# Optimization experiments

Measured on AMD Instinct MI355X. Metric: run time of the kernel, lower is better.

The kernel has to match this reference:

```python
import jax, jax.numpy as jnp
import numpy as np

V, E, H, K, B, T = 50000, 256, 256, 9, 128, 512


def lstm_dir(x, lens, Wih, Whh, b):
    # x: [B,T,E] -> h outputs [B,T,H], packed-sequence semantics:
    # state frozen and outputs zeroed for t >= lens[b].
    Bs, Ts, _ = x.shape
    Hh = Whh.shape[1]
    xw = jnp.einsum('bte,ge->btg', x, Wih) + b  # [B,T,4H] precomputed input proj
    valid = jnp.arange(Ts)[None, :] < lens[:, None]  # [B,T]

    def step(carry, inp):
        h, c = carry
        xw_t, v = inp  # [B,4H], [B]
        gates = xw_t + h @ Whh.T
        i, f, g, o = jnp.split(gates, 4, axis=-1)  # torch gate order i,f,g,o
        i = jax.nn.sigmoid(i)
        f = jax.nn.sigmoid(f)
        g = jnp.tanh(g)
        o = jax.nn.sigmoid(o)
        c_new = f * c + i * g
        h_new = o * jnp.tanh(c_new)
        v = v[:, None]
        return (jnp.where(v, h_new, h), jnp.where(v, c_new, c)), h_new * v

    init = (jnp.zeros((Bs, Hh), x.dtype), jnp.zeros((Bs, Hh), x.dtype))
    _, ys = jax.lax.scan(step, init, (jnp.swapaxes(xw, 0, 1), valid.T))
    return jnp.swapaxes(ys, 0, 1)


def reverse_by_len(x, lens):
    # per-row reversal within valid length; padding stays zero
    Ts = x.shape[1]
    t = jnp.arange(Ts)
    idx = jnp.clip(lens[:, None] - 1 - t[None, :], 0, Ts - 1)
    m = t[None, :] < lens[:, None]
    return jnp.take_along_axis(x, idx[:, :, None], axis=1) * m[:, :, None]


def crf_llh(em, tags, lens, start, end, trans):
    # torchcrf forward with reduction='sum': sum_b (gold score - logZ)
    Bs, Ts, Kk = em.shape
    mask = jnp.arange(Ts)[None, :] < lens[:, None]
    em_t = jnp.take_along_axis(em, tags[..., None], axis=-1)[..., 0]  # [B,T]
    score = start[tags[:, 0]] + em_t[:, 0]
    tr = trans[tags[:, :-1], tags[:, 1:]]  # [B,T-1]
    score = score + jnp.sum((tr + em_t[:, 1:]) * mask[:, 1:], axis=1)
    last_tag = jnp.take_along_axis(tags, (lens - 1)[:, None], axis=1)[:, 0]
    score = score + end[last_tag]

    def step(alpha, inp):
        e_t, m_t = inp  # [B,K], [B]
        nxt = jax.nn.logsumexp(alpha[:, :, None] + trans[None, :, :], axis=1) + e_t
        return jnp.where(m_t[:, None], nxt, alpha), None

    alpha0 = start[None, :] + em[:, 0]  # [B,K]
    alpha, _ = jax.lax.scan(step, alpha0,
                            (jnp.swapaxes(em[:, 1:], 0, 1), mask[:, 1:].T))
    logZ = jax.nn.logsumexp(alpha + end[None, :], axis=1)
    return jnp.sum(score - logZ)


def setup_inputs() -> dict:
    key = jax.random.key(0)
    ks = jax.random.split(key, 16)
    sentences = jax.random.randint(ks[0], (B, T), 0, V)
    tags = jax.random.randint(ks[1], (B, T), 0, K)
    length_list = jax.random.randint(ks[2], (B,), 1, T + 1)  # >=1 so mask[:,0] all true
    s = float(1.0 / np.sqrt(H))
    u = lambda k, sh: jax.random.uniform(k, sh, jnp.float32, -s, s)
    emb = jax.random.normal(ks[3], (V, E), jnp.float32) * float(np.sqrt(2.0 / E))
    return dict(
        sentences=sentences, tags=tags, length_list=length_list,
        emb=emb,
        Wih_f=u(ks[4], (4 * H, E)), Whh_f=u(ks[5], (4 * H, H)), b_f=u(ks[6], (4 * H,)),
        Wih_b=u(ks[7], (4 * H, E)), Whh_b=u(ks[8], (4 * H, H)), b_b=u(ks[9], (4 * H,)),
        W_out=u(ks[10], (K, 2 * H)), b_out=u(ks[11], (K,)),
        start=jax.random.uniform(ks[12], (K,), jnp.float32, -0.1, 0.1),
        end=jax.random.uniform(ks[13], (K,), jnp.float32, -0.1, 0.1),
        trans=jax.random.uniform(ks[14], (K, K), jnp.float32, -0.1, 0.1),
    )


def reference(sentences, tags, length_list, emb, Wih_f, Whh_f, b_f,
              Wih_b, Whh_b, b_b, W_out, b_out, start, end, trans):
    x = emb[sentences]  # [B,T,E]
    h_f = lstm_dir(x, length_list, Wih_f, Whh_f, b_f)
    x_rev = reverse_by_len(x, length_list)
    h_b = reverse_by_len(lstm_dir(x_rev, length_list, Wih_b, Whh_b, b_b), length_list)
    hcat = jnp.concatenate([h_f, h_b], axis=-1)  # [B,T,2H]
    # Dropout is identity in eval mode
    em = jnp.einsum('bth,kh->btk', hcat, W_out) + b_out  # [B,T,K]
    return crf_llh(em, tags, length_list, start, end, trans)
```

## Files before the change

kernel.cpp:

```cpp
#include <hip/hip_runtime.h>
#include <hip/hip_bf16.h>

typedef short v8s __attribute__((ext_vector_type(8)));
typedef int   v8i __attribute__((ext_vector_type(8)));
typedef float v4f __attribute__((ext_vector_type(4)));
typedef float v2f __attribute__((ext_vector_type(2)));

#define T_ 512

template<int HI>
__device__ __forceinline__ v2f cvt2(unsigned int wsrc){
  return __builtin_amdgcn_cvt_pk_f32_fp8((int)wsrc, HI);
}
__device__ __forceinline__ v2f rcp2(v2f d){
  return (v2f){__builtin_amdgcn_rcpf(d.x), __builtin_amdgcn_rcpf(d.y)};
}
__device__ __forceinline__ v2f tanh2(v2f x){
  v2f x2 = x*x;
  v2f num = x*(x2 + 27.f);
  v2f den = x2*9.f + 27.f;
  v2f r = num * rcp2(den);
  return (v2f){__builtin_amdgcn_fmed3f(r.x,-1.f,1.f),
               __builtin_amdgcn_fmed3f(r.y,-1.f,1.f)};
}
__device__ __forceinline__ v2f sigm2(v2f x){
  v2f y = x*0.5f;
  v2f y2 = y*y;
  v2f num = y*(y2 + 27.f);
  v2f den = y2*9.f + 27.f;
  v2f r = num * rcp2(den);
  v2f rc = (v2f){__builtin_amdgcn_fmed3f(r.x,-1.f,1.f),
                 __builtin_amdgcn_fmed3f(r.y,-1.f,1.f)};
  return rc*0.5f + 0.5f;
}
__device__ __forceinline__ int pi_col(int p){
  return ((p>>5)<<5) + ((p&1)<<4) + ((p&31)>>1);
}
__device__ __forceinline__ v8i ld32(const void* p){
  uint4 lo = *(const uint4*)p;
  uint4 hi = *(const uint4*)((const char*)p + 16);
  v8i r;
  r[0]=(int)lo.x; r[1]=(int)lo.y; r[2]=(int)lo.z; r[3]=(int)lo.w;
  r[4]=(int)hi.x; r[5]=(int)hi.y; r[6]=(int)hi.z; r[7]=(int)hi.w;
  return r;
}
__device__ __forceinline__ unsigned f2fp4(float x){
  unsigned s = (x < 0.f) ? 8u : 0u;
  float a = fabsf(x);
  unsigned m;
  if      (a < 0.25f) m=0u; else if (a < 0.75f) m=1u;
  else if (a < 1.25f) m=2u; else if (a < 1.75f) m=3u;
  else if (a < 2.5f ) m=4u; else if (a < 3.5f ) m=5u;
  else if (a < 5.f  ) m=6u; else m=7u;
  return s|m;
}
__device__ __forceinline__ unsigned pk8(float a, float b, float c, float d){
  int w = __builtin_amdgcn_cvt_pk_fp8_f32(a, b, 0, 0);
  w     = __builtin_amdgcn_cvt_pk_fp8_f32(c, d, w, 1);
  return (unsigned)w;
}
__device__ __forceinline__ unsigned enc4(v2f h){
  v2f t = h*4.f;
  unsigned b = 0;
  #pragma unroll
  for (int s=0;s<2;++s){
    float v = s ? t.y : t.x;
    float ax = __builtin_amdgcn_fmed3f(fabsf(v), 0.f, 4.f);
    float gl = fmaf(ax, 2.f, 12582912.f);
    float gh = ax + 12582912.f;
    unsigned ql = __builtin_bit_cast(unsigned, gl) & 7u;
    unsigned qh = (__builtin_bit_cast(unsigned, gh) & 7u) + 2u;
    unsigned c  = (ax > 1.75f) ? qh : ql;
    unsigned sg = (__builtin_bit_cast(unsigned, v) >> 28) & 8u;
    b |= (c | sg) << (4*s);
  }
  return b;
}

__global__ __launch_bounds__(256) void prep_wih8_k(
    const float* __restrict__ Wa, const float* __restrict__ Wb,
    unsigned char* __restrict__ out)
{
  int idx = blockIdx.x*256 + threadIdx.x;
  int lane = idx & 63;
  int t2 = idx >> 6;
  int ntile = t2 & 127;
  int kt = t2 >> 7;
  int n = ntile*16 + (lane&15);
  const float* W = (n < 1024) ? (Wa + (size_t)n*256) : (Wb + (size_t)(n-1024)*256);
  int k0 = kt*128 + (lane>>4)*32;
  unsigned words[8];
  #pragma unroll
  for (int e=0;e<8;++e)
    words[e] = pk8(W[k0+e*4], W[k0+e*4+1], W[k0+e*4+2], W[k0+e*4+3]);
  unsigned char* d = out + (size_t)idx*32;
  *(uint4*)(d)      = make_uint4(words[0], words[1], words[2], words[3]);
  *(uint4*)(d + 16) = make_uint4(words[4], words[5], words[6], words[7]);
}

__global__ __launch_bounds__(256) void prep_whh4_k(
    const float* __restrict__ Wf, const float* __restrict__ Wb,
    unsigned char* __restrict__ out)
{
  int idx = blockIdx.x*256 + threadIdx.x;
  int lane = idx & 63;
  int t2 = idx >> 6;
  int ntile = t2 & 63;
  int kt = (t2>>6) & 1;
  int dir = t2 >> 7;
  const float* W = dir ? Wb : Wf;
  int n = ntile*16 + (lane&15);
  int kbase = kt*128 + (lane>>4)*32;
  const float* row = W + (size_t)n*256;
  unsigned words[4];
  #pragma unroll
  for (int d4=0;d4<4;++d4){
    unsigned acc = 0;
    #pragma unroll
    for (int j=0;j<8;++j){
      float v = row[pi_col(kbase + d4*8 + j)] * 64.f;
      acc |= f2fp4(v) << (4*j);
    }
    words[d4] = acc;
  }
  *(uint4*)(out + (size_t)idx*16) = make_uint4(words[0], words[1], words[2], words[3]);
}

__global__ __launch_bounds__(256) void xw_gemm_k(
    const int* __restrict__ sent, const float* __restrict__ emb,
    const unsigned char* __restrict__ wihg, const int* __restrict__ lens,
    const float* __restrict__ bfv, const float* __restrict__ bbv,
    unsigned char* __restrict__ xw)
{
  int mt = blockIdx.x;
  if (((mt&3)<<7) >= lens[mt>>2]) return;
  __shared__ unsigned char A[128][272];
  int tid = threadIdx.x;
  {
    int row = tid>>1, half = tid&1;
    int tok = sent[mt*128 + row];
    const float4* s = (const float4*)(emb + (size_t)tok*256 + half*128);
    unsigned char* drow = &A[row][half*128];
    #pragma unroll
    for (int c4=0; c4<8; ++c4){
      unsigned w0[4];
      #pragma unroll
      for (int u=0; u<4; ++u){
        float4 v = s[c4*4+u];
        w0[u] = pk8(v.x, v.y, v.z, v.w);
      }
      *(uint4*)(drow + c4*16) = make_uint4(w0[0], w0[1], w0[2], w0[3]);
    }
  }
  __syncthreads();
  int w = tid>>6, lane = tid&63, lr = lane&15, lq = lane>>4;
  #pragma unroll 1
  for (int i4=0; i4<4; ++i4){
    int dnv = w*4 + i4;
    int dn = dnv>>3, v = dnv&7;
    const float* bb = dn ? bbv : bfv;
    float bias[8];
    #pragma unroll
    for (int e=0;e<8;++e){
      int q = e>>1, s = e&1;
      bias[e] = bb[q*256 + v*32 + s*16 + lr];
    }
    #pragma unroll 1
    for (int mh=0; mh<2; ++mh){
      v4f acc[8][4];
      #pragma unroll
      for (int e=0;e<8;++e)
        #pragma unroll
        for (int mm=0;mm<4;++mm) acc[e][mm] = (v4f){0.f,0.f,0.f,0.f};
      #pragma unroll
      for (int kt=0;kt<2;++kt){
        v8i a0 = ld32(&A[mh*64 +  0 + lr][kt*128 + lq*32]);
        v8i a1 = ld32(&A[mh*64 + 16 + lr][kt*128 + lq*32]);
        v8i a2 = ld32(&A[mh*64 + 32 + lr][kt*128 + lq*32]);
        v8i a3 = ld32(&A[mh*64 + 48 + lr][kt*128 + lq*32]);
        #pragma unroll
        for (int e=0;e<8;++e){
          int q = e>>1, s = e&1;
          int ntile = dn*64 + q*16 + v*2 + s;
          v8i bfr = ld32(wihg + ((size_t)(kt*128 + ntile)*64 + lane)*32);
          acc[e][0] = __builtin_amdgcn_mfma_scale_f32_16x16x128_f8f6f4(
                        a0, bfr, acc[e][0], 0,0, 0,0x7f7f7f7f, 0,0x7f7f7f7f);
          acc[e][1] = __builtin_amdgcn_mfma_scale_f32_16x16x128_f8f6f4(
                        a1, bfr, acc[e][1], 0,0, 0,0x7f7f7f7f, 0,0x7f7f7f7f);
          acc[e][2] = __builtin_amdgcn_mfma_scale_f32_16x16x128_f8f6f4(
                        a2, bfr, acc[e][2], 0,0, 0,0x7f7f7f7f, 0,0x7f7f7f7f);
          acc[e][3] = __builtin_amdgcn_mfma_scale_f32_16x16x128_f8f6f4(
                        a3, bfr, acc[e][3], 0,0, 0,0x7f7f7f7f, 0,0x7f7f7f7f);
        }
      }
      #pragma unroll
      for (int mm=0;mm<4;++mm){
        #pragma unroll
        for (int j=0;j<4;++j){
          int row = mt*128 + mh*64 + mm*16 + lq*4 + j;
          unsigned lo = pk8(acc[0][mm][j]+bias[0], acc[1][mm][j]+bias[1],
                            acc[2][mm][j]+bias[2], acc[3][mm][j]+bias[3]);
          unsigned hi = pk8(acc[4][mm][j]+bias[4], acc[5][mm][j]+bias[5],
                            acc[6][mm][j]+bias[6], acc[7][mm][j]+bias[7]);
          *(uint2*)(xw + ((size_t)dn*65536 + row)*1024 + v*128 + lr*8)
              = make_uint2(lo, hi);
        }
      }
    }
  }
}

__global__ __launch_bounds__(512,1) void lstm_k(
    const unsigned char* __restrict__ xw,
    const unsigned char* __restrict__ whh4,
    const int* __restrict__ lens,
    unsigned char* __restrict__ hout)
{
  int bid = blockIdx.x, dir = bid>>5, grp = bid&31;
  int tid = threadIdx.x, w = tid>>6, lane = tid&63, lr = lane&15, lq = lane>>4;
  __shared__ unsigned char hbuf[2][16][136];
  __shared__ int tmax_s;
  for (int i=tid*4; i<2*16*136; i+=512*4) *(unsigned int*)(&((unsigned char*)hbuf)[i]) = 0u;
  if (tid==0){
    int mx=0;
    for (int i=0;i<4;++i){ int l = lens[grp*4+i]; mx = l>mx? l:mx; }
    tmax_s = mx;
  }
  v8i wreg[16];
  const unsigned char* wb = whh4 + (size_t)dir*131072;
  #pragma unroll
  for (int kt=0;kt<2;++kt){
    #pragma unroll
    for (int nt=0;nt<8;++nt){
      int ntile = (nt>>1)*16 + w*2 + (nt&1);
      uint4 t = *(const uint4*)(wb + ((size_t)(kt*64 + ntile)*64 + lane)*16);
      v8i r;
      r[0]=(int)t.x; r[1]=(int)t.y; r[2]=(int)t.z; r[3]=(int)t.w;
      r[4]=0; r[5]=0; r[6]=0; r[7]=0;
      wreg[kt*8+nt] = r;
    }
  }
  int seq = grp*4 + lq;
  int ln = lens[seq];
  v2f cc = (v2f){0.f, 0.f};
  const size_t dbase = (size_t)dir*65536;
  const unsigned char* xbase = xw + (dbase + (size_t)seq*T_)*1024 + w*128 + lr*8;
  unsigned char* hbase = hout + (dbase + (size_t)seq*T_)*256 + w*32 + lr*2;
  unsigned char* lw0 = &hbuf[1][lq*4][w*16 + lr];
  unsigned char* lw1 = &hbuf[0][lq*4][w*16 + lr];
  const unsigned char* lr0 = &hbuf[0][lr][lq*16];
  const unsigned char* lr1 = &hbuf[1][lr][lq*16];
  __syncthreads();
  int tmax = tmax_s;
  uint2 xv = *(const uint2*)(xbase + (size_t)(dir ? (ln-1) : 0)*1024);

  #define STEP_BODY(TE_EXPR, POS_EXPR)                                         \
    int cur = t&1;                                                             \
    int tn = (t+1<tmax)? t+1 : t;                                              \
    int te = (TE_EXPR);                                                        \
    uint2 xn = *(const uint2*)(xbase + ((size_t)te<<10));                      \
    const unsigned char* lrd = cur? lr1 : lr0;                                 \
    v2f xi = cvt2<0>(xv.x), xf = cvt2<1>(xv.x);                                \
    v2f xg = cvt2<0>(xv.y), xo = cvt2<1>(xv.y);                                \
    v4f acc[8];                                                                \
    _Pragma("unroll")                                                          \
    for (int nt=0;nt<8;++nt) asm("" : "=v"(acc[nt]));                          \
    acc[0][0] = xi.x; acc[1][0] = xi.y;                                        \
    acc[2][0] = xf.x; acc[3][0] = xf.y;                                        \
    acc[4][0] = xg.x; acc[5][0] = xg.y;                                        \
    acc[6][0] = xo.x; acc[7][0] = xo.y;                                        \
    _Pragma("unroll")                                                          \
    for (int kt=0;kt<2;++kt){                                                  \
      uint4 hh = *(const uint4*)(lrd + kt*64);                                 \
      v8i a;                                                                   \
      a[0]=(int)hh.x; a[1]=(int)hh.y; a[2]=(int)hh.z; a[3]=(int)hh.w;          \
      a[4]=0; a[5]=0; a[6]=0; a[7]=0;                                          \
      _Pragma("unroll")                                                        \
      for (int nt=0;nt<8;++nt)                                                 \
        acc[nt] = __builtin_amdgcn_mfma_scale_f32_16x16x128_f8f6f4(            \
                    a, wreg[kt*8+nt], acc[nt], 4, 4,                           \
                    0, 0x7D7D7D7D, 0, 0x79797979);                             \
    }                                                                          \
    int pos = (POS_EXPR);                                                      \
    v2f gi = (v2f){acc[0][0], acc[1][0]};                                      \
    v2f gf = (v2f){acc[2][0], acc[3][0]};                                      \
    v2f gg = (v2f){acc[4][0], acc[5][0]};                                      \
    v2f go = (v2f){acc[6][0], acc[7][0]};                                      \
    v2f iv = sigm2(gi), fv = sigm2(gf), gv = tanh2(gg), ov = sigm2(go);        \
    v2f cn = fv*cc + iv*gv;                                                    \
    v2f hn = ov*tanh2(cn);                                                     \
    cc = cn;                                                                   \
    int hp = __builtin_amdgcn_cvt_pk_fp8_f32(hn.x, hn.y, 0, 0);                \
    *(unsigned short*)(hbase + ((size_t)pos<<8)) = (unsigned short)(hp&0xffff);\
    *(cur? lw1 : lw0) = (unsigned char)enc4(hn);                               \
    xv = xn;                                                                   \
    asm volatile("s_waitcnt lgkmcnt(0)" ::: "memory");                         \
    __builtin_amdgcn_s_barrier();                                              \
    __builtin_amdgcn_sched_barrier(0);

  if (dir == 0){
    for (int t=0; t<tmax; ++t){
      STEP_BODY(tn, t)
    }
  } else {
    for (int t=0; t<tmax; ++t){
      STEP_BODY((tn<ln)? (ln-1-tn) : tn, (t<ln)? (ln-1-t) : t)
    }
  }
  #undef STEP_BODY
}

__global__ __launch_bounds__(256) void em_k(
    const unsigned char* __restrict__ hout,
    const float* __restrict__ Wout, const float* __restrict__ bout,
    const int* __restrict__ lens,
    float* __restrict__ em)
{
  __shared__ float Ws[9*512];
  for (int i=threadIdx.x;i<9*512;i+=256){
    int k = i>>9, p = i&511;
    int d = p>>8, pp = p&255;
    Ws[i] = Wout[k*512 + d*256 + pi_col(pp)];
  }
  __syncthreads();
  int wv = blockIdx.x*4 + (threadIdx.x>>6);
  int lane = threadIdx.x & 63;
  int g = lane>>4, r = lane&15;
  int m = wv*4 + g;
  const unsigned char* hf = hout + (size_t)m*256 + r*16;
  const unsigned char* hb = hout + ((size_t)65536 + m)*256 + r*16;
  uint4 vf = *(const uint4*)hf;
  uint4 vb = *(const uint4*)hb;
  float xf[16], xb[16];
  {
    v2f d0=cvt2<0>(vf.x), d1=cvt2<1>(vf.x), d2=cvt2<0>(vf.y), d3=cvt2<1>(vf.y);
    v2f d4=cvt2<0>(vf.z), d5=cvt2<1>(vf.z), d6=cvt2<0>(vf.w), d7=cvt2<1>(vf.w);
    xf[0]=d0.x; xf[1]=d0.y; xf[2]=d1.x; xf[3]=d1.y;
    xf[4]=d2.x; xf[5]=d2.y; xf[6]=d3.x; xf[7]=d3.y;
    xf[8]=d4.x; xf[9]=d4.y; xf[10]=d5.x; xf[11]=d5.y;
    xf[12]=d6.x; xf[13]=d6.y; xf[14]=d7.x; xf[15]=d7.y;
  }
  {
    v2f d0=cvt2<0>(vb.x), d1=cvt2<1>(vb.x), d2=cvt2<0>(vb.y), d3=cvt2<1>(vb.y);
    v2f d4=cvt2<0>(vb.z), d5=cvt2<1>(vb.z), d6=cvt2<0>(vb.w), d7=cvt2<1>(vb.w);
    xb[0]=d0.x; xb[1]=d0.y; xb[2]=d1.x; xb[3]=d1.y;
    xb[4]=d2.x; xb[5]=d2.y; xb[6]=d3.x; xb[7]=d3.y;
    xb[8]=d4.x; xb[9]=d4.y; xb[10]=d5.x; xb[11]=d5.y;
    xb[12]=d6.x; xb[13]=d6.y; xb[14]=d7.x; xb[15]=d7.y;
  }
  float a[9];
  #pragma unroll
  for (int k=0;k<9;++k){
    float s = 0.f;
    #pragma unroll
    for (int e=0;e<16;++e)
      s += xf[e]*Ws[k*512 + r*16 + e] + xb[e]*Ws[k*512 + 256 + r*16 + e];
    a[k]=s;
  }
  #pragma unroll
  for (int k=0;k<9;++k){
    #pragma unroll
    for (int off=8; off; off>>=1) a[k] += __shfl_xor(a[k], off, 64);
  }
  int b = m>>9, t = m&511;
  if (r==0 && t < lens[b]){
    float* d = em + (size_t)m*9;
    #pragma unroll
    for (int k=0;k<9;++k) d[k] = a[k] + bout[k];
  }
}

__global__ __launch_bounds__(256) void crf_k(
    const float* __restrict__ em, const int* __restrict__ tags,
    const int* __restrict__ lens, const float* __restrict__ startv,
    const float* __restrict__ endv, const float* __restrict__ trans,
    float* __restrict__ out)
{
  int wid = blockIdx.x*4 + (threadIdx.x>>6);
  int lane = threadIdx.x & 63;
  const float* e = em + (size_t)wid*T_*9;
  const int* tg = tags + (size_t)wid*T_;
  int L = lens[wid];
  float p = 0.f;
  for (int t = 1+lane; t < L; t += 64)
    p += trans[tg[t-1]*9 + tg[t]] + e[(size_t)t*9 + tg[t]];
  if (lane==0) p += startv[tg[0]] + e[tg[0]] + endv[tg[L-1]];
  #pragma unroll
  for (int off=32; off; off>>=1) p += __shfl_xor(p, off, 64);
  float tcol[9];
  #pragma unroll
  for (int i=0;i<9;++i) tcol[i] = (lane<9) ? trans[i*9 + lane] : 0.f;
  float alpha = (lane<9) ? (startv[lane] + e[lane]) : -1e30f;
  for (int t=1; t<L; ++t){
    float vs[9]; float mx = -1e30f;
    #pragma unroll
    for (int i=0;i<9;++i){
      float ai = __shfl(alpha, i, 64);
      vs[i] = ai + tcol[i];
      mx = fmaxf(mx, vs[i]);
    }
    float s = 0.f;
    #pragma unroll
    for (int i=0;i<9;++i) s += __expf(vs[i]-mx);
    float na = mx + __logf(s) + ((lane<9)? e[(size_t)t*9+lane] : 0.f);
    alpha = (lane<9) ? na : -1e30f;
  }
  float v = (lane<9) ? (alpha + endv[lane]) : -1e30f;
  float mx = v;
  #pragma unroll
  for (int off=32; off; off>>=1) mx = fmaxf(mx, __shfl_xor(mx, off, 64));
  float s = __expf(v-mx);
  #pragma unroll
  for (int off=32; off; off>>=1) s += __shfl_xor(s, off, 64);
  float logZ = mx + __logf(s);
  if (lane==0) atomicAdd(out, p - logZ);
}

extern "C" void kernel_launch(void* const* d_in, const int* in_sizes, int n_in,
                              void* d_out, int out_size, void* d_ws, size_t ws_size,
                              hipStream_t stream)
{
  const int*   sent  = (const int*)d_in[0];
  const int*   tags  = (const int*)d_in[1];
  const int*   lens  = (const int*)d_in[2];
  const float* emb   = (const float*)d_in[3];
  const float* Wih_f = (const float*)d_in[4];
  const float* Whh_f = (const float*)d_in[5];
  const float* b_f   = (const float*)d_in[6];
  const float* Wih_b = (const float*)d_in[7];
  const float* Whh_b = (const float*)d_in[8];
  const float* b_b   = (const float*)d_in[9];
  const float* Wout  = (const float*)d_in[10];
  const float* bout  = (const float*)d_in[11];
  const float* startv= (const float*)d_in[12];
  const float* endv  = (const float*)d_in[13];
  const float* trans = (const float*)d_in[14];
  char* ws = (char*)d_ws;
  unsigned char* wihg8 = (unsigned char*)(ws);
  unsigned char* whh4  = (unsigned char*)(ws + (size_t)524288);
  unsigned char* xw    = (unsigned char*)(ws + (size_t)1048576);
  unsigned char* hout  = (unsigned char*)(ws + (size_t)135266304);
  float* em            = (float*)(ws + (size_t)168820736);
  float* outp = (float*)d_out;

  (void)hipMemsetAsync(outp, 0, sizeof(float), stream);
  prep_wih8_k<<<64, 256, 0, stream>>>(Wih_f, Wih_b, wihg8);
  prep_whh4_k<<<64, 256, 0, stream>>>(Whh_f, Whh_b, whh4);
  xw_gemm_k<<<512, 256, 0, stream>>>(sent, emb, wihg8, lens, b_f, b_b, xw);
  lstm_k<<<64, 512, 0, stream>>>(xw, whh4, lens, hout);
  em_k<<<4096, 256, 0, stream>>>(hout, Wout, bout, lens, em);
  crf_k<<<32, 256, 0, stream>>>(em, tags, lens, startv, endv, trans, outp);
}
```

Baseline: 704.5 us.

## Merge weight prep kernels, reorder LSTM MFMAs, scalarize gates, early-exit em_k

The two weight-quantization kernels are merged into one launch to save a kernel launch. In the LSTM step loop, both h loads are hoisted and the MFMA chain is reordered so even and odd accumulator tiles are processed separately. Gate activations become scalar per unit so the first unit's gates and state write can start before the odd tiles finish, shortening the serial critical path. The h byte now goes to shared memory before the global store, and em_k returns early for whole waves past the sequence length.

```diff
diff --git a/kernel.cpp b/kernel.cpp
--- a/kernel.cpp
+++ b/kernel.cpp
@@ -33,6 +33,14 @@
                  __builtin_amdgcn_fmed3f(r.y,-1.f,1.f)};
   return rc*0.5f + 0.5f;
 }
+__device__ __forceinline__ float tanh1(float x){
+  float x2 = x*x;
+  float r = (x*(27.f + x2)) * __builtin_amdgcn_rcpf(27.f + 9.f*x2);
+  return __builtin_amdgcn_fmed3f(r, -1.f, 1.f);
+}
+__device__ __forceinline__ float sigm1(float x){
+  return 0.5f + 0.5f*tanh1(0.5f*x);
+}
 __device__ __forceinline__ int pi_col(int p){
   return ((p>>5)<<5) + ((p&1)<<4) + ((p&31)>>1);
 }
@@ -59,71 +67,63 @@
   w     = __builtin_amdgcn_cvt_pk_fp8_f32(c, d, w, 1);
   return (unsigned)w;
 }
-__device__ __forceinline__ unsigned enc4(v2f h){
-  v2f t = h*4.f;
-  unsigned b = 0;
-  #pragma unroll
-  for (int s=0;s<2;++s){
-    float v = s ? t.y : t.x;
-    float ax = __builtin_amdgcn_fmed3f(fabsf(v), 0.f, 4.f);
-    float gl = fmaf(ax, 2.f, 12582912.f);
-    float gh = ax + 12582912.f;
-    unsigned ql = __builtin_bit_cast(unsigned, gl) & 7u;
-    unsigned qh = (__builtin_bit_cast(unsigned, gh) & 7u) + 2u;
-    unsigned c  = (ax > 1.75f) ? qh : ql;
-    unsigned sg = (__builtin_bit_cast(unsigned, v) >> 28) & 8u;
-    b |= (c | sg) << (4*s);
-  }
-  return b;
-}
-
-__global__ __launch_bounds__(256) void prep_wih8_k(
-    const float* __restrict__ Wa, const float* __restrict__ Wb,
-    unsigned char* __restrict__ out)
-{
-  int idx = blockIdx.x*256 + threadIdx.x;
-  int lane = idx & 63;
-  int t2 = idx >> 6;
-  int ntile = t2 & 127;
-  int kt = t2 >> 7;
-  int n = ntile*16 + (lane&15);
-  const float* W = (n < 1024) ? (Wa + (size_t)n*256) : (Wb + (size_t)(n-1024)*256);
-  int k0 = kt*128 + (lane>>4)*32;
-  unsigned words[8];
-  #pragma unroll
-  for (int e=0;e<8;++e)
-    words[e] = pk8(W[k0+e*4], W[k0+e*4+1], W[k0+e*4+2], W[k0+e*4+3]);
-  unsigned char* d = out + (size_t)idx*32;
-  *(uint4*)(d)      = make_uint4(words[0], words[1], words[2], words[3]);
-  *(uint4*)(d + 16) = make_uint4(words[4], words[5], words[6], words[7]);
-}
-
-__global__ __launch_bounds__(256) void prep_whh4_k(
-    const float* __restrict__ Wf, const float* __restrict__ Wb,
-    unsigned char* __restrict__ out)
-{
-  int idx = blockIdx.x*256 + threadIdx.x;
-  int lane = idx & 63;
-  int t2 = idx >> 6;
-  int ntile = t2 & 63;
-  int kt = (t2>>6) & 1;
-  int dir = t2 >> 7;
-  const float* W = dir ? Wb : Wf;
-  int n = ntile*16 + (lane&15);
-  int kbase = kt*128 + (lane>>4)*32;
-  const float* row = W + (size_t)n*256;
-  unsigned words[4];
-  #pragma unroll
-  for (int d4=0;d4<4;++d4){
-    unsigned acc = 0;
-    #pragma unroll
-    for (int j=0;j<8;++j){
-      float v = row[pi_col(kbase + d4*8 + j)] * 64.f;
-      acc |= f2fp4(v) << (4*j);
-    }
-    words[d4] = acc;
-  }
-  *(uint4*)(out + (size_t)idx*16) = make_uint4(words[0], words[1], words[2], words[3]);
+__device__ __forceinline__ unsigned enc4s(float v4x){
+  float ax = __builtin_amdgcn_fmed3f(fabsf(v4x), 0.f, 4.f);
+  float gl = fmaf(ax, 2.f, 12582912.f);
+  float gh = ax + 12582912.f;
+  unsigned ql = __builtin_bit_cast(unsigned, gl) & 7u;
+  unsigned qh = (__builtin_bit_cast(unsigned, gh) & 7u) + 2u;
+  unsigned c  = (ax > 1.75f) ? qh : ql;
+  unsigned sg = (__builtin_bit_cast(unsigned, v4x) >> 28) & 8u;
+  return c | sg;
+}
+
+__global__ __launch_bounds__(256) void prep_k(
+    const float* __restrict__ WihA, const float* __restrict__ WihB,
+    const float* __restrict__ WhhF, const float* __restrict__ WhhB,
+    unsigned char* __restrict__ wih_out, unsigned char* __restrict__ whh_out)
+{
+  int blk = blockIdx.x;
+  if (blk < 64){
+    int idx = blk*256 + threadIdx.x;
+    int lane = idx & 63;
+    int t2 = idx >> 6;
+    int ntile = t2 & 127;
+    int kt = t2 >> 7;
+    int n = ntile*16 + (lane&15);
+    const float* W = (n < 1024) ? (WihA + (size_t)n*256) : (WihB + (size_t)(n-1024)*256);
+    int k0 = kt*128 + (lane>>4)*32;
+    unsigned words[8];
+    #pragma unroll
+    for (int e=0;e<8;++e)
+      words[e] = pk8(W[k0+e*4], W[k0+e*4+1], W[k0+e*4+2], W[k0+e*4+3]);
+    unsigned char* d = wih_out + (size_t)idx*32;
+    *(uint4*)(d)      = make_uint4(words[0], words[1], words[2], words[3]);
+    *(uint4*)(d + 16) = make_uint4(words[4], words[5], words[6], words[7]);
+  } else {
+    int idx = (blk-64)*256 + threadIdx.x;
+    int lane = idx & 63;
+    int t2 = idx >> 6;
+    int ntile = t2 & 63;
+    int kt = (t2>>6) & 1;
+    int dir = t2 >> 7;
+    const float* W = dir ? WhhB : WhhF;
+    int n = ntile*16 + (lane&15);
+    int kbase = kt*128 + (lane>>4)*32;
+    const float* row = W + (size_t)n*256;
+    unsigned words[4];
+    #pragma unroll
+    for (int d4=0;d4<4;++d4){
+      unsigned acc = 0;
+      #pragma unroll
+      for (int j=0;j<8;++j){
+        float v = row[pi_col(kbase + d4*8 + j)] * 64.f;
+        acc |= f2fp4(v) << (4*j);
+      }
+      words[d4] = acc;
+    }
+    *(uint4*)(whh_out + (size_t)idx*16) = make_uint4(words[0], words[1], words[2], words[3]);
+  }
 }
 
 __global__ __launch_bounds__(256) void xw_gemm_k(
@@ -242,7 +242,7 @@
   }
   int seq = grp*4 + lq;
   int ln = lens[seq];
-  v2f cc = (v2f){0.f, 0.f};
+  float c0 = 0.f, c1 = 0.f;
   const size_t dbase = (size_t)dir*65536;
   const unsigned char* xbase = xw + (dbase + (size_t)seq*T_)*1024 + w*128 + lr*8;
   unsigned char* hbase = hout + (dbase + (size_t)seq*T_)*256 + w*32 + lr*2;
@@ -269,30 +269,46 @@
     acc[2][0] = xf.x; acc[3][0] = xf.y;                                        \
     acc[4][0] = xg.x; acc[5][0] = xg.y;                                        \
     acc[6][0] = xo.x; acc[7][0] = xo.y;                                        \
+    uint4 hh0 = *(const uint4*)(lrd);                                          \
+    uint4 hh1 = *(const uint4*)(lrd + 64);                                     \
+    v8i a0;                                                                    \
+    a0[0]=(int)hh0.x; a0[1]=(int)hh0.y; a0[2]=(int)hh0.z; a0[3]=(int)hh0.w;    \
+    a0[4]=0; a0[5]=0; a0[6]=0; a0[7]=0;                                        \
+    v8i a1;                                                                    \
+    a1[0]=(int)hh1.x; a1[1]=(int)hh1.y; a1[2]=(int)hh1.z; a1[3]=(int)hh1.w;    \
+    a1[4]=0; a1[5]=0; a1[6]=0; a1[7]=0;                                        \
+                                          \
     _Pragma("unroll")                                                          \
-    for (int kt=0;kt<2;++kt){                                                  \
-      uint4 hh = *(const uint4*)(lrd + kt*64);                                 \
-      v8i a;                                                                   \
-      a[0]=(int)hh.x; a[1]=(int)hh.y; a[2]=(int)hh.z; a[3]=(int)hh.w;          \
-      a[4]=0; a[5]=0; a[6]=0; a[7]=0;                                          \
-      _Pragma("unroll")                                                        \
-      for (int nt=0;nt<8;++nt)                                                 \
-        acc[nt] = __builtin_amdgcn_mfma_scale_f32_16x16x128_f8f6f4(            \
-                    a, wreg[kt*8+nt], acc[nt], 4, 4,                           \
-                    0, 0x7D7D7D7D, 0, 0x79797979);                             \
+    for (int nt=0;nt<8;nt+=2){                                                 \
+      acc[nt] = __builtin_amdgcn_mfma_scale_f32_16x16x128_f8f6f4(              \
+                  a0, wreg[nt], acc[nt], 4, 4, 0, 0x7D7D7D7D, 0, 0x79797979);  \
+      acc[nt] = __builtin_amdgcn_mfma_scale_f32_16x16x128_f8f6f4(              \
+                  a1, wreg[8+nt], acc[nt], 4, 4, 0, 0x7D7D7D7D, 0, 0x79797979);\
     }                                                                          \
+               \
+    _Pragma("unroll")                                                          \
+    for (int nt=1;nt<8;nt+=2){                                                 \
+      acc[nt] = __builtin_amdgcn_mfma_scale_f32_16x16x128_f8f6f4(              \
+                  a0, wreg[nt], acc[nt], 4, 4, 0, 0x7D7D7D7D, 0, 0x79797979);  \
+      acc[nt] = __builtin_amdgcn_mfma_scale_f32_16x16x128_f8f6f4(              \
+                  a1, wreg[8+nt], acc[nt], 4, 4, 0, 0x7D7D7D7D, 0, 0x79797979);\
+    }                                                                          \
+    float iv0 = sigm1(acc[0][0]), fv0 = sigm1(acc[2][0]);                      \
+    float gv0 = tanh1(acc[4][0]), ov0 = sigm1(acc[6][0]);                      \
+    float cn0 = fv0*c0 + iv0*gv0;                                              \
+    float hn0 = ov0*tanh1(cn0);                                                \
+    c0 = cn0;                                                                  \
+    unsigned e0 = enc4s(hn0*4.f);                                              \
+    float iv1 = sigm1(acc[1][0]), fv1 = sigm1(acc[3][0]);                      \
+    float gv1 = tanh1(acc[5][0]), ov1 = sigm1(acc[7][0]);                      \
+    float cn1 = fv1*c1 + iv1*gv1;                                              \
+    float hn1 = ov1*tanh1(cn1);                                                \
+    c1 = cn1;                                                                  \
+    unsigned e1 = enc4s(hn1*4.f);                                              \
     int pos = (POS_EXPR);                                                      \
-    v2f gi = (v2f){acc[0][0], acc[1][0]};                                      \
-    v2f gf = (v2f){acc[2][0], acc[3][0]};                                      \
-    v2f gg = (v2f){acc[4][0], acc[5][0]};                                      \
-    v2f go = (v2f){acc[6][0], acc[7][0]};                                      \
-    v2f iv = sigm2(gi), fv = sigm2(gf), gv = tanh2(gg), ov = sigm2(go);        \
-    v2f cn = fv*cc + iv*gv;                                                    \
-    v2f hn = ov*tanh2(cn);                                                     \
-    cc = cn;                                                                   \
-    int hp = __builtin_amdgcn_cvt_pk_fp8_f32(hn.x, hn.y, 0, 0);                \
+    *(cur? lw1 : lw0) = (unsigned char)(e0 | (e1<<4));                         \
+    int hp = __builtin_amdgcn_cvt_pk_fp8_f32(hn0, hn1, 0, 0);                  \
     *(unsigned short*)(hbase + ((size_t)pos<<8)) = (unsigned short)(hp&0xffff);\
-    *(cur? lw1 : lw0) = (unsigned char)enc4(hn);                               \
     xv = xn;                                                                   \
     asm volatile("s_waitcnt lgkmcnt(0)" ::: "memory");                         \
     __builtin_amdgcn_s_barrier();                                              \
@@ -326,7 +342,11 @@
   int wv = blockIdx.x*4 + (threadIdx.x>>6);
   int lane = threadIdx.x & 63;
   int g = lane>>4, r = lane&15;
-  int m = wv*4 + g;
+  int m4 = wv*4;
+  int b = m4>>9, t0 = m4&511;
+  int len = lens[b];
+  if (t0 >= len) return;
+  int m = m4 + g;
   const unsigned char* hf = hout + (size_t)m*256 + r*16;
   const unsigned char* hb = hout + ((size_t)65536 + m)*256 + r*16;
   uint4 vf = *(const uint4*)hf;
@@ -362,8 +382,8 @@
     #pragma unroll
     for (int off=8; off; off>>=1) a[k] += __shfl_xor(a[k], off, 64);
   }
-  int b = m>>9, t = m&511;
-  if (r==0 && t < lens[b]){
+  int t = m&511;
+  if (r==0 && t < len){
     float* d = em + (size_t)m*9;
     #pragma unroll
     for (int k=0;k<9;++k) d[k] = a[k] + bout[k];
@@ -444,8 +464,7 @@
   float* outp = (float*)d_out;
 
   (void)hipMemsetAsync(outp, 0, sizeof(float), stream);
-  prep_wih8_k<<<64, 256, 0, stream>>>(Wih_f, Wih_b, wihg8);
-  prep_whh4_k<<<64, 256, 0, stream>>>(Whh_f, Whh_b, whh4);
+  prep_k<<<128, 256, 0, stream>>>(Wih_f, Wih_b, Whh_f, Whh_b, wihg8, whh4);
   xw_gemm_k<<<512, 256, 0, stream>>>(sent, emb, wihg8, lens, b_f, b_b, xw);
   lstm_k<<<64, 512, 0, stream>>>(xw, whh4, lens, hout);
   em_k<<<4096, 256, 0, stream>>>(hout, Wout, bout, lens, em);
```

Result: no change. 697.0 us (-1.1%).
